# Optimization experiments

Measured on AMD Instinct MI355X. Metric: run time of the kernel, lower is better.

Reference implementation:

```python
import jax, jax.numpy as jnp
import numpy as np

D_MODEL = 1024
D_STATE = 16
D_CONV = 4
EXPAND = 2
DT_RANK = 64
D_INNER = EXPAND * D_MODEL
B, L = 1, 2048


def setup_inputs() -> dict:
    key = jax.random.key(0)
    ks = jax.random.split(key, 10)
    x = jax.random.normal(ks[0], (B, L, D_MODEL), dtype=jnp.float32)
    # linear weights (stored as [out, in], like torch)
    W_in = jax.random.normal(ks[1], (2 * D_INNER, D_MODEL), dtype=jnp.float32) * (1.0 / np.sqrt(D_MODEL))
    conv_w = jax.random.normal(ks[2], (D_INNER, 1, D_CONV), dtype=jnp.float32) * (1.0 / np.sqrt(D_CONV))
    conv_b = jax.random.normal(ks[3], (D_INNER,), dtype=jnp.float32) * 0.02
    W_x = jax.random.normal(ks[4], (DT_RANK + 2 * D_STATE, D_INNER), dtype=jnp.float32) * (1.0 / np.sqrt(D_INNER))
    W_dt = jax.random.normal(ks[5], (D_INNER, DT_RANK), dtype=jnp.float32) * (1.0 / np.sqrt(DT_RANK))
    # dt bias init: inverse-softplus of dt ~ LogUniform(1e-3, 0.1)
    dt = jnp.exp(jax.random.uniform(ks[6], (D_INNER,)) * (np.log(0.1) - np.log(0.001)) + np.log(0.001))
    dt = jnp.clip(dt, 1e-4, None)
    b_dt = dt + jnp.log(-jnp.expm1(-dt))
    # A_log init: log(1..d_state) broadcast over d_inner
    A_log = jnp.log(jnp.broadcast_to(jnp.arange(1, D_STATE + 1, dtype=jnp.float32)[None, :], (D_INNER, D_STATE)))
    D_param = jnp.ones((D_INNER,), dtype=jnp.float32)
    W_out = jax.random.normal(ks[7], (D_MODEL, D_INNER), dtype=jnp.float32) * (1.0 / np.sqrt(D_INNER))
    return dict(x=x, W_in=W_in, conv_w=conv_w, conv_b=conv_b, W_x=W_x,
                W_dt=W_dt, b_dt=b_dt, A_log=A_log, D_param=D_param, W_out=W_out)


def _silu(v):
    return v * jax.nn.sigmoid(v)


def _mamba_forward(x, W_in, conv_w, conv_b, W_x, W_dt, b_dt, A_log, D_param, W_out):
    # in_proj: (B, L, 2*d_inner)
    xz = jnp.einsum('bld,ed->ble', x, W_in)
    x_in, z = jnp.split(xz, 2, axis=-1)  # each (B, L, d_inner)

    # depthwise causal conv1d (torch pads d_conv-1 both sides then truncates -> causal left pad)
    xc = jnp.transpose(x_in, (0, 2, 1))  # (B, d_inner, L)
    xc = jax.lax.conv_general_dilated(
        xc, conv_w,
        window_strides=(1,), padding=[(D_CONV - 1, 0)],
        dimension_numbers=('NCH', 'OIH', 'NCH'),
        feature_group_count=D_INNER)
    xc = xc + conv_b[None, :, None]
    x_conv = _silu(jnp.transpose(xc, (0, 2, 1)))  # (B, L, d_inner)

    # selective SSM
    A = -jnp.exp(A_log)  # (d_inner, d_state)
    x_dbl = jnp.einsum('bld,ed->ble', x_conv, W_x)  # (B, L, dt_rank + 2*d_state)
    dt_low, B_ssm, C = jnp.split(x_dbl, [DT_RANK, DT_RANK + D_STATE], axis=-1)
    dt = jax.nn.softplus(jnp.einsum('blr,dr->bld', dt_low, W_dt) + b_dt)  # (B, L, d_inner)

    dA = jnp.exp(jnp.einsum('bld,dn->bldn', dt, A))                        # (B, L, d_inner, d_state)
    dBx = dt[..., None] * B_ssm[:, :, None, :] * x_conv[..., None]          # dB * x, (B, L, d_inner, d_state)

    def step(h, inp):
        dA_t, dBx_t, C_t = inp          # (B, d, n), (B, d, n), (B, n)
        h = dA_t * h + dBx_t
        y_t = jnp.einsum('bdn,bn->bd', h, C_t)
        return h, y_t

    h0 = jnp.zeros((x.shape[0], D_INNER, D_STATE), dtype=x.dtype)
    xs = (jnp.swapaxes(dA, 0, 1), jnp.swapaxes(dBx, 0, 1), jnp.swapaxes(C, 0, 1))
    _, ys = jax.lax.scan(step, h0, xs)   # ys: (L, B, d_inner)
    y = jnp.swapaxes(ys, 0, 1) + x_conv * D_param  # (B, L, d_inner)

    y = y * _silu(z)
    return jnp.einsum('bld,ed->ble', y, W_out)  # (B, L, d_model)


def reference(x, W_in, conv_w, conv_b, W_x, W_dt, b_dt, A_log, D_param, W_out):
    return _mamba_forward(x, W_in, conv_w, conv_b, W_x, W_dt, b_dt, A_log, D_param, W_out)
```

## Files before the change

kernel.cpp:

```cpp
#include <hip/hip_runtime.h>
#include <math.h>

#define LSEQ   2048
#define DMODEL 1024
#define DINNER 2048
#define DSTATE 16
#define DTRANK 64
#define XCOLS  96
#define CL     32
#define NC     (LSEQ/CL)
#define SSTATE (DINNER*DSTATE)

typedef __attribute__((ext_vector_type(8))) short bf16x8;
typedef __attribute__((ext_vector_type(4))) float f32x4;
typedef unsigned short ushort_t;
typedef unsigned int uint_t;

__device__ __forceinline__ float siluf(float v) { return v / (1.f + __expf(-v)); }

__device__ __forceinline__ ushort_t f2bf(float f) {
    uint_t u = __float_as_uint(f);
    u += 0x7FFFu + ((u >> 16) & 1u);
    return (ushort_t)(u >> 16);
}
__device__ __forceinline__ float bf2f(ushort_t u) {
    return __uint_as_float((uint_t)u << 16);
}

__device__ __forceinline__ bf16x8 cvt8(float4 lo, float4 hi) {
    bf16x8 r;
    r[0] = (short)f2bf(lo.x); r[1] = (short)f2bf(lo.y);
    r[2] = (short)f2bf(lo.z); r[3] = (short)f2bf(lo.w);
    r[4] = (short)f2bf(hi.x); r[5] = (short)f2bf(hi.y);
    r[6] = (short)f2bf(hi.z); r[7] = (short)f2bf(hi.w);
    return r;
}

__global__ __launch_bounds__(256)
void cast6_kernel(const float* __restrict__ s0, ushort_t* __restrict__ d0, int c0,
                  const float* __restrict__ s1, ushort_t* __restrict__ d1, int c1,
                  const float* __restrict__ s2, ushort_t* __restrict__ d2, int c2,
                  const float* __restrict__ s3, ushort_t* __restrict__ d3, int c3,
                  const float* __restrict__ s4, ushort_t* __restrict__ d4, int c4,
                  float* __restrict__ z0, int cz)
{
    int i = (blockIdx.x * 256 + threadIdx.x) * 8;
    int tot = c0 + c1 + c2 + c3 + c4;
    if (i < tot) {
        const float* s; ushort_t* d;
        if (i < c0)                { s = s0 + i;                  d = d0 + i; }
        else if (i < c0+c1)        { s = s1 + (i-c0);             d = d1 + (i-c0); }
        else if (i < c0+c1+c2)     { s = s2 + (i-c0-c1);          d = d2 + (i-c0-c1); }
        else if (i < c0+c1+c2+c3)  { s = s3 + (i-c0-c1-c2);       d = d3 + (i-c0-c1-c2); }
        else                       { s = s4 + (i-c0-c1-c2-c3);    d = d4 + (i-c0-c1-c2-c3); }
        *(bf16x8*)d = cvt8(*(const float4*)s, *(const float4*)(s + 4));
    } else if (i < tot + cz) {
        float* z = z0 + (i - tot);
        *(float4*)z       = make_float4(0.f, 0.f, 0.f, 0.f);
        *(float4*)(z + 4) = make_float4(0.f, 0.f, 0.f, 0.f);
    }
}

__device__ __forceinline__ void stage_tile(const ushort_t* __restrict__ A,
                                           const ushort_t* __restrict__ B,
                                           ushort_t* As, ushort_t* Bs,
                                           int m0, int n0, int K, int k0, int tid)
{
#pragma unroll
    for (int j = 0; j < 2; j++) {
        const int c   = j * 256 + tid;
        const int row = c & 127;
        const int kbi = c >> 7;
        __builtin_amdgcn_global_load_lds(
            (const __attribute__((address_space(1))) uint_t*)(A + (size_t)(m0 + row) * K + k0 + kbi * 8),
            (__attribute__((address_space(3))) uint_t*)((char*)As + c * 16), 16, 0, 0);
        __builtin_amdgcn_global_load_lds(
            (const __attribute__((address_space(1))) uint_t*)(B + (size_t)(n0 + row) * K + k0 + kbi * 8),
            (__attribute__((address_space(3))) uint_t*)((char*)Bs + c * 16), 16, 0, 0);
    }
}

template<int EPI, int SPLITK>
__global__ __launch_bounds__(256)
void gemm_bf16(const ushort_t* __restrict__ A,
               const ushort_t* __restrict__ B,
               float* __restrict__ C,
               ushort_t* __restrict__ Xb,
               ushort_t* __restrict__ Gz,
               int M, int N, int K, size_t partStride)
{
    __shared__ ushort_t As[2][4096];
    __shared__ ushort_t Bs[2][4096];

    const int tid  = threadIdx.x;
    const int wid  = tid >> 6;
    const int lane = tid & 63;
    const int m0 = blockIdx.x * 128;
    const int n0 = blockIdx.y * 128;
    const int kcnt  = K / SPLITK;
    const int kbase = (SPLITK > 1) ? blockIdx.z * kcnt : 0;
    const int NT = kcnt / 32;
    float* Cp = (EPI == 0) ? C + (size_t)blockIdx.z * partStride : C;
    const int wr = (wid >> 1) * 64;
    const int wc = (wid & 1) * 64;
    const int lr = lane & 15;
    const int kbq = lane >> 4;

    f32x4 acc[4][4];
#pragma unroll
    for (int m = 0; m < 4; m++)
#pragma unroll
        for (int n = 0; n < 4; n++)
            acc[m][n] = (f32x4){0.f, 0.f, 0.f, 0.f};

    stage_tile(A, B, As[0], Bs[0], m0, n0, K, kbase, tid);

    for (int t = 0; t < NT; t++) {
        const int cur = t & 1;
        if (t + 1 < NT) {
            stage_tile(A, B, As[cur ^ 1], Bs[cur ^ 1], m0, n0, K, kbase + (t + 1) * 32, tid);
            asm volatile("s_waitcnt vmcnt(4)" ::: "memory");
        } else {
            asm volatile("s_waitcnt vmcnt(0)" ::: "memory");
        }
        __builtin_amdgcn_s_barrier();
        __builtin_amdgcn_sched_barrier(0);

        bf16x8 af[4], bfr[4];
#pragma unroll
        for (int m = 0; m < 4; m++)
            af[m] = *(const bf16x8*)&As[cur][(kbq * 128 + wr + m * 16 + lr) * 8];
#pragma unroll
        for (int n = 0; n < 4; n++)
            bfr[n] = *(const bf16x8*)&Bs[cur][(kbq * 128 + wc + n * 16 + lr) * 8];
#pragma unroll
        for (int m = 0; m < 4; m++)
#pragma unroll
            for (int n = 0; n < 4; n++)
                acc[m][n] = __builtin_amdgcn_mfma_f32_16x16x32_bf16(af[m], bfr[n], acc[m][n], 0, 0, 0);

        __builtin_amdgcn_sched_barrier(0);
        __builtin_amdgcn_s_barrier();
    }

    const int er = (lane >> 4) * 4;
    const int ec = lane & 15;
    if (EPI == 0) {
#pragma unroll
        for (int m = 0; m < 4; m++) {
            const int grow = m0 + wr + m * 16 + er;
#pragma unroll
            for (int n = 0; n < 4; n++) {
                const int gcol = n0 + wc + n * 16 + ec;
#pragma unroll
                for (int r = 0; r < 4; r++)
                    Cp[(size_t)(grow + r) * N + gcol] = acc[m][n][r];
            }
        }
    } else {
        const bool xside = (n0 < DINNER);
#pragma unroll
        for (int m = 0; m < 4; m++) {
            const int grow = m0 + wr + m * 16 + er;
#pragma unroll
            for (int n = 0; n < 4; n++) {
                const int gcol = n0 + wc + n * 16 + ec;
#pragma unroll
                for (int r = 0; r < 4; r++) {
                    float v = acc[m][n][r];
                    if (xside)
                        Xb[(size_t)(grow + r) * DINNER + gcol] = f2bf(v);
                    else
                        Gz[(size_t)(grow + r) * DINNER + (gcol - DINNER)] = f2bf(siluf(v));
                }
            }
        }
    }
}

__global__ __launch_bounds__(256)
void add2_kernel(const float* __restrict__ p0, const float* __restrict__ p1,
                 float* __restrict__ out, int n)
{
    int i = (blockIdx.x * 256 + threadIdx.x) * 4;
    if (i >= n) return;
    float4 a = *(const float4*)(p0 + i);
    float4 b = *(const float4*)(p1 + i);
    *(float4*)(out + i) = make_float4(a.x + b.x, a.y + b.y, a.z + b.z, a.w + b.w);
}

__global__ __launch_bounds__(256)
void gemm_xdbl(const ushort_t* __restrict__ A,
               const ushort_t* __restrict__ B,
               float* __restrict__ Cout)
{
    const int tid = threadIdx.x, wid = tid >> 6, lane = tid & 63;
    const int m0 = blockIdx.x * 128;
    const int kbase = blockIdx.z * 128;
    const int wr = (wid >> 1) * 64;
    const int wc = (wid & 1) * 48;
    const int lr = lane & 15;
    const int kq = (lane >> 4) * 8;

    f32x4 acc[4][3];
#pragma unroll
    for (int m = 0; m < 4; m++)
#pragma unroll
        for (int n = 0; n < 3; n++)
            acc[m][n] = (f32x4){0.f, 0.f, 0.f, 0.f};

#pragma unroll
    for (int ks = 0; ks < 4; ks++) {
        const int k0 = kbase + ks * 32;
        bf16x8 af[4], bfr[3];
#pragma unroll
        for (int m = 0; m < 4; m++)
            af[m] = *(const bf16x8*)(A + (size_t)(m0 + wr + m * 16 + lr) * DINNER + k0 + kq);
#pragma unroll
        for (int n = 0; n < 3; n++)
            bfr[n] = *(const bf16x8*)(B + (size_t)(wc + n * 16 + lr) * DINNER + k0 + kq);
#pragma unroll
        for (int m = 0; m < 4; m++)
#pragma unroll
            for (int n = 0; n < 3; n++)
                acc[m][n] = __builtin_amdgcn_mfma_f32_16x16x32_bf16(af[m], bfr[n], acc[m][n], 0, 0, 0);
    }

    const int er = (lane >> 4) * 4;
    const int ec = lane & 15;
#pragma unroll
    for (int m = 0; m < 4; m++)
#pragma unroll
        for (int n = 0; n < 3; n++)
#pragma unroll
            for (int r = 0; r < 4; r++)
                atomicAdd(&Cout[(size_t)(m0 + wr + m * 16 + er + r) * XCOLS + wc + n * 16 + ec],
                          acc[m][n][r]);
}

__global__ __launch_bounds__(256)
void gemm_dt(const float* __restrict__ Axd,
             const ushort_t* __restrict__ Bw,
             const float* __restrict__ bias,
             ushort_t* __restrict__ dtmb)
{
    const int tid = threadIdx.x, wid = tid >> 6, lane = tid & 63;
    const int m0 = blockIdx.x * 128;
    const int n0 = blockIdx.y * 128;
    const int wr = (wid >> 1) * 64;
    const int wc = (wid & 1) * 64;
    const int lr = lane & 15;
    const int kq = (lane >> 4) * 8;

    f32x4 acc[4][4];
#pragma unroll
    for (int m = 0; m < 4; m++)
#pragma unroll
        for (int n = 0; n < 4; n++)
            acc[m][n] = (f32x4){0.f, 0.f, 0.f, 0.f};

#pragma unroll
    for (int kk = 0; kk < 2; kk++) {
        bf16x8 af[4], bfr[4];
#pragma unroll
        for (int m = 0; m < 4; m++) {
            const float* p = Axd + (size_t)(m0 + wr + m * 16 + lr) * XCOLS + kk * 32 + kq;
            af[m] = cvt8(*(const float4*)p, *(const float4*)(p + 4));
        }
#pragma unroll
        for (int n = 0; n < 4; n++)
            bfr[n] = *(const bf16x8*)(Bw + (size_t)(n0 + wc + n * 16 + lr) * DTRANK + kk * 32 + kq);
#pragma unroll
        for (int m = 0; m < 4; m++)
#pragma unroll
            for (int n = 0; n < 4; n++)
                acc[m][n] = __builtin_amdgcn_mfma_f32_16x16x32_bf16(af[m], bfr[n], acc[m][n], 0, 0, 0);
    }

    const int er = (lane >> 4) * 4;
    const int ec = lane & 15;
#pragma unroll
    for (int m = 0; m < 4; m++)
#pragma unroll
        for (int n = 0; n < 4; n++) {
            const int gcol = n0 + wc + n * 16 + ec;
            const float bv = bias[gcol];
#pragma unroll
            for (int r = 0; r < 4; r++) {
                float c = acc[m][n][r] + bv;
                c = (c > 20.f) ? c : log1pf(__expf(c));
                dtmb[(size_t)(m0 + wr + m * 16 + er + r) * DINNER + gcol] = f2bf(c);
            }
        }
}

__global__ __launch_bounds__(256)
void conv_silu_kernel(const ushort_t* __restrict__ xinb,
                      const float* __restrict__ conv_w,
                      const float* __restrict__ conv_b,
                      ushort_t* __restrict__ xcb)
{
    int idx = blockIdx.x * 256 + threadIdx.x;
    if (idx >= LSEQ * DINNER) return;
    int t = idx / DINNER;
    int d = idx - t * DINNER;
    float acc = conv_b[d];
#pragma unroll
    for (int j = 0; j < 4; j++) {
        int tt = t - 3 + j;
        if (tt >= 0)
            acc = fmaf(conv_w[d*4 + j], bf2f(xinb[(size_t)tt * DINNER + d]), acc);
    }
    xcb[idx] = f2bf(siluf(acc));
}

__global__ __launch_bounds__(256)
void scan_phase1(const ushort_t* __restrict__ dtmb,
                 const float* __restrict__ xdbl,
                 const ushort_t* __restrict__ xcb,
                 const float* __restrict__ A_log,
                 float* __restrict__ Aprod, float* __restrict__ hend)
{
    __shared__ float Bs[CL][16];
    const int tid = threadIdx.x;
    const int d = blockIdx.x * 256 + tid;
    const int c = blockIdx.y;
    const int t0 = c * CL;

    {
        int t = tid >> 3, n = (tid * 2) & 15;
        float2 v = *(const float2*)&xdbl[(size_t)(t0 + t) * XCOLS + DTRANK + n];
        Bs[t][n] = v.x; Bs[t][n + 1] = v.y;
    }

    float a[16];
#pragma unroll
    for (int q = 0; q < 4; q++) {
        f32x4 v = *(const f32x4*)&A_log[(size_t)d * DSTATE + q * 4];
#pragma unroll
        for (int j = 0; j < 4; j++) a[q * 4 + j] = -__expf(v[j]);
    }
    float h[16];
#pragma unroll
    for (int n = 0; n < 16; n++) h[n] = 0.f;
    float sdt = 0.f;

    __syncthreads();

    float dtv = bf2f(dtmb[(size_t)t0 * DINNER + d]);
    float xv  = bf2f(xcb[(size_t)t0 * DINNER + d]);
    for (int tt = 0; tt < CL; tt++) {
        int tn_ = t0 + ((tt + 1 < CL) ? tt + 1 : tt);
        float dtv_n = bf2f(dtmb[(size_t)tn_ * DINNER + d]);
        float xv_n  = bf2f(xcb[(size_t)tn_ * DINNER + d]);

        f32x4 Bq[4];
#pragma unroll
        for (int q = 0; q < 4; q++) Bq[q] = *(const f32x4*)&Bs[tt][q * 4];
        float dtx = dtv * xv;
        sdt += dtv;
#pragma unroll
        for (int n = 0; n < 16; n++) {
            float e = __expf(dtv * a[n]);
            h[n] = fmaf(e, h[n], dtx * Bq[n >> 2][n & 3]);
        }
        dtv = dtv_n; xv = xv_n;
    }

#pragma unroll
    for (int n = 0; n < 16; n++) {
        const size_t k = (size_t)c * SSTATE + (size_t)n * DINNER + d;
        hend[k]  = h[n];
        Aprod[k] = __expf(a[n] * sdt);
    }
}

__global__ __launch_bounds__(256)
void scan_phase2(const float* __restrict__ Aprod, float* __restrict__ hend)
{
    const int idx = blockIdx.x * 256 + threadIdx.x;
    float carry = 0.f;
#pragma unroll
    for (int c = 0; c < NC; c++) {
        const size_t k = (size_t)c * SSTATE + idx;
        float oh = hend[k];
        float oA = Aprod[k];
        hend[k] = carry;
        carry = fmaf(oA, carry, oh);
    }
}

__global__ __launch_bounds__(256)
void scan_phase3(const ushort_t* __restrict__ dtmb,
                 const float* __restrict__ xdbl,
                 const ushort_t* __restrict__ xcb,
                 const float* __restrict__ A_log,
                 const float* __restrict__ Dp,
                 const ushort_t* __restrict__ gz,
                 const float* __restrict__ hinit,
                 ushort_t* __restrict__ yb)
{
    __shared__ float Bs[CL][16];
    __shared__ float Cs[CL][16];
    const int tid = threadIdx.x;
    const int d = blockIdx.x * 256 + tid;
    const int c = blockIdx.y;
    const int t0 = c * CL;

    {
        int r = tid & 127;
        int t = r >> 2, n = (r * 4) & 15;
        const float* src = &xdbl[(size_t)(t0 + t) * XCOLS + DTRANK + ((tid < 128) ? 0 : DSTATE) + n];
        float4 v = *(const float4*)src;
        float* dst = (tid < 128) ? &Bs[t][n] : &Cs[t][n];
        dst[0] = v.x; dst[1] = v.y; dst[2] = v.z; dst[3] = v.w;
    }

    float a[16];
#pragma unroll
    for (int q = 0; q < 4; q++) {
        f32x4 v = *(const f32x4*)&A_log[(size_t)d * DSTATE + q * 4];
#pragma unroll
        for (int j = 0; j < 4; j++) a[q * 4 + j] = -__expf(v[j]);
    }
    const float Dv = Dp[d];
    float h[16];
#pragma unroll
    for (int n = 0; n < 16; n++)
        h[n] = hinit[(size_t)c * SSTATE + (size_t)n * DINNER + d];

    __syncthreads();

    float dtv = bf2f(dtmb[(size_t)t0 * DINNER + d]);
    float xv  = bf2f(xcb[(size_t)t0 * DINNER + d]);
    for (int tt = 0; tt < CL; tt++) {
        const int t = t0 + tt;
        int tn_ = t0 + ((tt + 1 < CL) ? tt + 1 : tt);
        float dtv_n = bf2f(dtmb[(size_t)tn_ * DINNER + d]);
        float xv_n  = bf2f(xcb[(size_t)tn_ * DINNER + d]);
        float gzv   = bf2f(gz[(size_t)t * DINNER + d]);

        f32x4 Bq[4], Cq[4];
#pragma unroll
        for (int q = 0; q < 4; q++) {
            Bq[q] = *(const f32x4*)&Bs[tt][q * 4];
            Cq[q] = *(const f32x4*)&Cs[tt][q * 4];
        }
        float dtx = dtv * xv;
        float y = 0.f;
#pragma unroll
        for (int n = 0; n < 16; n++) {
            float e = __expf(dtv * a[n]);
            h[n] = fmaf(e, h[n], dtx * Bq[n >> 2][n & 3]);
            y = fmaf(h[n], Cq[n >> 2][n & 3], y);
        }
        yb[(size_t)t * DINNER + d] = f2bf((y + Dv * xv) * gzv);
        dtv = dtv_n; xv = xv_n;
    }
}

extern "C" void kernel_launch(void* const* d_in, const int* in_sizes, int n_in,
                              void* d_out, int out_size, void* d_ws, size_t ws_size,
                              hipStream_t stream)
{
    const float* x      = (const float*)d_in[0];
    const float* W_in   = (const float*)d_in[1];
    const float* conv_w = (const float*)d_in[2];
    const float* conv_b = (const float*)d_in[3];
    const float* W_x    = (const float*)d_in[4];
    const float* W_dt   = (const float*)d_in[5];
    const float* b_dt   = (const float*)d_in[6];
    const float* A_log  = (const float*)d_in[7];
    const float* D_par  = (const float*)d_in[8];
    const float* W_out  = (const float*)d_in[9];
    float* out = (float*)d_out;
    float* ws  = (float*)d_ws;

    float* xdbl  = ws;
    float* Aprod = xdbl + (size_t)LSEQ * XCOLS;
    float* hend  = Aprod + (size_t)NC * SSTATE;
    ushort_t* xb   = (ushort_t*)(hend + (size_t)NC * SSTATE);
    ushort_t* Wib  = xb   + (size_t)LSEQ * DMODEL;
    ushort_t* Wob  = Wib  + (size_t)(2*DINNER) * DMODEL;
    ushort_t* Wxb  = Wob  + (size_t)DMODEL * DINNER;
    ushort_t* Wdtb = Wxb  + (size_t)XCOLS * DINNER;
    ushort_t* xinb = Wdtb + (size_t)DINNER * DTRANK;
    ushort_t* gz   = xinb + (size_t)LSEQ * DINNER;
    ushort_t* xcb  = gz   + (size_t)LSEQ * DINNER;
    ushort_t* dtmb = xcb  + (size_t)LSEQ * DINNER;
    ushort_t* yb   = dtmb + (size_t)LSEQ * DINNER;
    float* outp = (float*)xcb;

    {
        int c0 = LSEQ * DMODEL, c1 = 2 * DINNER * DMODEL, c2 = DMODEL * DINNER;
        int c3 = XCOLS * DINNER, c4 = DINNER * DTRANK;
        int cz = LSEQ * XCOLS;
        int total = c0 + c1 + c2 + c3 + c4 + cz;
        hipLaunchKernelGGL(cast6_kernel, dim3((total / 8 + 255) / 256), dim3(256), 0, stream,
                           x, xb, c0, W_in, Wib, c1, W_out, Wob, c2,
                           W_x, Wxb, c3, W_dt, Wdtb, c4, xdbl, cz);
    }

    hipLaunchKernelGGL((gemm_bf16<1,1>), dim3(LSEQ/128, (2*DINNER)/128), dim3(256), 0, stream,
                       xb, Wib, (float*)nullptr, xinb, gz, LSEQ, 2*DINNER, DMODEL, (size_t)0);

    hipLaunchKernelGGL(conv_silu_kernel, dim3((LSEQ*DINNER)/256), dim3(256), 0, stream,
                       xinb, conv_w, conv_b, xcb);

    hipLaunchKernelGGL(gemm_xdbl, dim3(LSEQ/128, 1, 16), dim3(256), 0, stream,
                       xcb, Wxb, xdbl);

    hipLaunchKernelGGL(gemm_dt, dim3(LSEQ/128, DINNER/128), dim3(256), 0, stream,
                       xdbl, Wdtb, b_dt, dtmb);

    hipLaunchKernelGGL(scan_phase1, dim3(DINNER/256, NC), dim3(256), 0, stream,
                       dtmb, xdbl, xcb, A_log, Aprod, hend);
    hipLaunchKernelGGL(scan_phase2, dim3(SSTATE/256), dim3(256), 0, stream,
                       Aprod, hend);
    hipLaunchKernelGGL(scan_phase3, dim3(DINNER/256, NC), dim3(256), 0, stream,
                       dtmb, xdbl, xcb, A_log, D_par, gz, hend, yb);

    hipLaunchKernelGGL((gemm_bf16<0,2>), dim3(LSEQ/128, DMODEL/128, 2), dim3(256), 0, stream,
                       yb, Wob, outp, (ushort_t*)nullptr, (ushort_t*)nullptr,
                       LSEQ, DMODEL, DINNER, (size_t)(LSEQ*DMODEL));
    hipLaunchKernelGGL(add2_kernel, dim3((LSEQ*DMODEL/4)/256), dim3(256), 0, stream,
                       outp, outp + (size_t)LSEQ*DMODEL, out, LSEQ*DMODEL);
}
```

Baseline: 200.0 us.

## Parallelize chunk-carry scan with warp shuffles, lengthen chunks, split-K out_proj by four

Doubles the scan chunk length to 64, which halves the number of chunks to 32. The inter-chunk carry pass changes from a serial per-state loop into a 32-lane warp shuffle scan over packed (A, h) float2 pairs. The output projection switches from split-K=2 to split-K=4 with a generic partial-sum reduction kernel, and its partials move to the xinb buffer. The aim is more parallelism in phase 2 and the out GEMM, at the cost of longer serial loops per thread in phases 1 and 3 and more partial-sum traffic.

```diff
diff --git a/kernel.cpp b/kernel.cpp
--- a/kernel.cpp
+++ b/kernel.cpp
@@ -7,7 +7,7 @@
 #define DSTATE 16
 #define DTRANK 64
 #define XCOLS  96
-#define CL     32
+#define CL     64
 #define NC     (LSEQ/CL)
 #define SSTATE (DINNER*DSTATE)
 
@@ -178,15 +178,19 @@
     }
 }
 
-__global__ __launch_bounds__(256)
-void add2_kernel(const float* __restrict__ p0, const float* __restrict__ p1,
-                 float* __restrict__ out, int n)
+template<int NP>
+__global__ __launch_bounds__(256)
+void addp_kernel(const float* __restrict__ parts, float* __restrict__ out, int n)
 {
     int i = (blockIdx.x * 256 + threadIdx.x) * 4;
     if (i >= n) return;
-    float4 a = *(const float4*)(p0 + i);
-    float4 b = *(const float4*)(p1 + i);
-    *(float4*)(out + i) = make_float4(a.x + b.x, a.y + b.y, a.z + b.z, a.w + b.w);
+    float4 s = *(const float4*)(parts + i);
+#pragma unroll
+    for (int p = 1; p < NP; p++) {
+        float4 v = *(const float4*)(parts + (size_t)p * n + i);
+        s.x += v.x; s.y += v.y; s.z += v.z; s.w += v.w;
+    }
+    *(float4*)(out + i) = s;
 }
 
 __global__ __launch_bounds__(256)
@@ -319,7 +323,7 @@
                  const float* __restrict__ xdbl,
                  const ushort_t* __restrict__ xcb,
                  const float* __restrict__ A_log,
-                 float* __restrict__ Aprod, float* __restrict__ hend)
+                 float2* __restrict__ state)
 {
     __shared__ float Bs[CL][16];
     const int tid = threadIdx.x;
@@ -328,9 +332,9 @@
     const int t0 = c * CL;
 
     {
-        int t = tid >> 3, n = (tid * 2) & 15;
-        float2 v = *(const float2*)&xdbl[(size_t)(t0 + t) * XCOLS + DTRANK + n];
-        Bs[t][n] = v.x; Bs[t][n + 1] = v.y;
+        int t = tid >> 2, n = (tid & 3) * 4;
+        float4 v = *(const float4*)&xdbl[(size_t)(t0 + t) * XCOLS + DTRANK + n];
+        Bs[t][n] = v.x; Bs[t][n+1] = v.y; Bs[t][n+2] = v.z; Bs[t][n+3] = v.w;
     }
 
     float a[16];
@@ -368,26 +372,28 @@
     }
 
 #pragma unroll
-    for (int n = 0; n < 16; n++) {
-        const size_t k = (size_t)c * SSTATE + (size_t)n * DINNER + d;
-        hend[k]  = h[n];
-        Aprod[k] = __expf(a[n] * sdt);
-    }
-}
-
-__global__ __launch_bounds__(256)
-void scan_phase2(const float* __restrict__ Aprod, float* __restrict__ hend)
-{
-    const int idx = blockIdx.x * 256 + threadIdx.x;
-    float carry = 0.f;
-#pragma unroll
-    for (int c = 0; c < NC; c++) {
-        const size_t k = (size_t)c * SSTATE + idx;
-        float oh = hend[k];
-        float oA = Aprod[k];
-        hend[k] = carry;
-        carry = fmaf(oA, carry, oh);
-    }
+    for (int n = 0; n < 16; n++)
+        state[(size_t)c * SSTATE + (size_t)n * DINNER + d] =
+            make_float2(__expf(a[n] * sdt), h[n]);
+}
+
+__global__ __launch_bounds__(256)
+void scan_phase2(float2* __restrict__ state)
+{
+    const int lane32 = threadIdx.x & 31;
+    const int chain  = blockIdx.x * 8 + (threadIdx.x >> 5);
+    const size_t off = (size_t)lane32 * SSTATE + chain;
+    float2 s = state[off];
+    float A = s.x, h = s.y;
+#pragma unroll
+    for (int dlt = 1; dlt < 32; dlt <<= 1) {
+        float Ap = __shfl_up(A, dlt, 32);
+        float hp = __shfl_up(h, dlt, 32);
+        if (lane32 >= dlt) { h = fmaf(A, hp, h); A = A * Ap; }
+    }
+    float carry = __shfl_up(h, 1, 32);
+    if (lane32 == 0) carry = 0.f;
+    ((float*)&state[off])[1] = carry;
 }
 
 __global__ __launch_bounds__(256)
@@ -397,7 +403,7 @@
                  const float* __restrict__ A_log,
                  const float* __restrict__ Dp,
                  const ushort_t* __restrict__ gz,
-                 const float* __restrict__ hinit,
+                 const float2* __restrict__ state,
                  ushort_t* __restrict__ yb)
 {
     __shared__ float Bs[CL][16];
@@ -409,11 +415,13 @@
 
     {
         int r = tid & 127;
-        int t = r >> 2, n = (r * 4) & 15;
-        const float* src = &xdbl[(size_t)(t0 + t) * XCOLS + DTRANK + ((tid < 128) ? 0 : DSTATE) + n];
-        float4 v = *(const float4*)src;
-        float* dst = (tid < 128) ? &Bs[t][n] : &Cs[t][n];
-        dst[0] = v.x; dst[1] = v.y; dst[2] = v.z; dst[3] = v.w;
+        int t = r >> 1, nb = (r & 1) * 8;
+        const float* src = &xdbl[(size_t)(t0 + t) * XCOLS + DTRANK + ((tid < 128) ? 0 : DSTATE) + nb];
+        float* dst = (tid < 128) ? &Bs[t][nb] : &Cs[t][nb];
+        float4 v0 = *(const float4*)src;
+        float4 v1 = *(const float4*)(src + 4);
+        dst[0]=v0.x; dst[1]=v0.y; dst[2]=v0.z; dst[3]=v0.w;
+        dst[4]=v1.x; dst[5]=v1.y; dst[6]=v1.z; dst[7]=v1.w;
     }
 
     float a[16];
@@ -427,7 +435,7 @@
     float h[16];
 #pragma unroll
     for (int n = 0; n < 16; n++)
-        h[n] = hinit[(size_t)c * SSTATE + (size_t)n * DINNER + d];
+        h[n] = state[(size_t)c * SSTATE + (size_t)n * DINNER + d].y;
 
     __syncthreads();
 
@@ -476,10 +484,9 @@
     float* out = (float*)d_out;
     float* ws  = (float*)d_ws;
 
-    float* xdbl  = ws;
-    float* Aprod = xdbl + (size_t)LSEQ * XCOLS;
-    float* hend  = Aprod + (size_t)NC * SSTATE;
-    ushort_t* xb   = (ushort_t*)(hend + (size_t)NC * SSTATE);
+    float*  xdbl  = ws;
+    float2* state = (float2*)(xdbl + (size_t)LSEQ * XCOLS);
+    ushort_t* xb   = (ushort_t*)(state + (size_t)NC * SSTATE);
     ushort_t* Wib  = xb   + (size_t)LSEQ * DMODEL;
     ushort_t* Wob  = Wib  + (size_t)(2*DINNER) * DMODEL;
     ushort_t* Wxb  = Wob  + (size_t)DMODEL * DINNER;
@@ -489,7 +496,7 @@
     ushort_t* xcb  = gz   + (size_t)LSEQ * DINNER;
     ushort_t* dtmb = xcb  + (size_t)LSEQ * DINNER;
     ushort_t* yb   = dtmb + (size_t)LSEQ * DINNER;
-    float* outp = (float*)xcb;
+    float* outp = (float*)xinb;
 
     {
         int c0 = LSEQ * DMODEL, c1 = 2 * DINNER * DMODEL, c2 = DMODEL * DINNER;
@@ -514,15 +521,15 @@
                        xdbl, Wdtb, b_dt, dtmb);
 
     hipLaunchKernelGGL(scan_phase1, dim3(DINNER/256, NC), dim3(256), 0, stream,
-                       dtmb, xdbl, xcb, A_log, Aprod, hend);
-    hipLaunchKernelGGL(scan_phase2, dim3(SSTATE/256), dim3(256), 0, stream,
-                       Aprod, hend);
+                       dtmb, xdbl, xcb, A_log, state);
+    hipLaunchKernelGGL(scan_phase2, dim3(SSTATE/8), dim3(256), 0, stream,
+                       state);
     hipLaunchKernelGGL(scan_phase3, dim3(DINNER/256, NC), dim3(256), 0, stream,
-                       dtmb, xdbl, xcb, A_log, D_par, gz, hend, yb);
-
-    hipLaunchKernelGGL((gemm_bf16<0,2>), dim3(LSEQ/128, DMODEL/128, 2), dim3(256), 0, stream,
+                       dtmb, xdbl, xcb, A_log, D_par, gz, state, yb);
+
+    hipLaunchKernelGGL((gemm_bf16<0,4>), dim3(LSEQ/128, DMODEL/128, 4), dim3(256), 0, stream,
                        yb, Wob, outp, (ushort_t*)nullptr, (ushort_t*)nullptr,
                        LSEQ, DMODEL, DINNER, (size_t)(LSEQ*DMODEL));
-    hipLaunchKernelGGL(add2_kernel, dim3((LSEQ*DMODEL/4)/256), dim3(256), 0, stream,
-                       outp, outp + (size_t)LSEQ*DMODEL, out, LSEQ*DMODEL);
-}
+    hipLaunchKernelGGL((addp_kernel<4>), dim3((LSEQ*DMODEL/4)/256), dim3(256), 0, stream,
+                       outp, out, LSEQ*DMODEL);
+}
```

After: 211.6 us. 1.06x slower.

## Stage GEMM epilogues through LDS for vector stores; interleave scan chunk state

Applied to the files above, without the earlier changes.

The in_proj and dt GEMM epilogues now write bf16 results into swizzled shared memory, then read them back as 8-element rows so global writes are wide, coalesced 16-byte stores instead of scattered 2-byte stores. The separate Aprod and hend arrays for the chunked scan are merged into one interleaved float2 state array, so phase 2 does one 8-byte load per chunk. The out_proj partial buffer is moved onto xinb. The gemm_dt epilogue also keeps a redundant scalar store of zero before each vector store, which adds write traffic. The extra shared-memory round trip and __syncthreads add a small cost per tile.

```diff
diff --git a/kernel.cpp b/kernel.cpp
--- a/kernel.cpp
+++ b/kernel.cpp
@@ -159,21 +159,32 @@
         }
     } else {
         const bool xside = (n0 < DINNER);
-#pragma unroll
-        for (int m = 0; m < 4; m++) {
-            const int grow = m0 + wr + m * 16 + er;
-#pragma unroll
-            for (int n = 0; n < 4; n++) {
-                const int gcol = n0 + wc + n * 16 + ec;
+        ushort_t* eps = (wid < 2) ? As[wid] : Bs[wid - 2];
+#pragma unroll
+        for (int m = 0; m < 4; m++)
+#pragma unroll
+            for (int n = 0; n < 4; n++)
 #pragma unroll
                 for (int r = 0; r < 4; r++) {
+                    const int rl = m * 16 + er + r;
+                    const int cl = n * 16 + ec;
                     float v = acc[m][n][r];
-                    if (xside)
-                        Xb[(size_t)(grow + r) * DINNER + gcol] = f2bf(v);
-                    else
-                        Gz[(size_t)(grow + r) * DINNER + (gcol - DINNER)] = f2bf(siluf(v));
+                    eps[rl * 64 + (cl ^ ((rl & 7) * 8))] =
+                        xside ? f2bf(v) : f2bf(siluf(v));
                 }
-            }
+        __syncthreads();
+        const int row8 = lane >> 3;
+        const int c8   = (lane & 7) * 8;
+#pragma unroll
+        for (int p = 0; p < 8; p++) {
+            const int rl = p * 8 + row8;
+            bf16x8 v = *(const bf16x8*)&eps[rl * 64 + (c8 ^ ((rl & 7) * 8))];
+            const int grow = m0 + wr + rl;
+            const int gcol = n0 + wc + c8;
+            if (xside)
+                *(bf16x8*)(Xb + (size_t)grow * DINNER + gcol) = v;
+            else
+                *(bf16x8*)(Gz + (size_t)grow * DINNER + (gcol - DINNER)) = v;
         }
     }
 }
@@ -244,6 +255,7 @@
              const float* __restrict__ bias,
              ushort_t* __restrict__ dtmb)
 {
+    __shared__ ushort_t eps4[4][4096];
     const int tid = threadIdx.x, wid = tid >> 6, lane = tid & 63;
     const int m0 = blockIdx.x * 128;
     const int n0 = blockIdx.y * 128;
@@ -279,19 +291,31 @@
 
     const int er = (lane >> 4) * 4;
     const int ec = lane & 15;
+    ushort_t* eps = eps4[wid];
 #pragma unroll
     for (int m = 0; m < 4; m++)
 #pragma unroll
         for (int n = 0; n < 4; n++) {
-            const int gcol = n0 + wc + n * 16 + ec;
-            const float bv = bias[gcol];
+            const int cl = n * 16 + ec;
+            const float bv = bias[n0 + wc + cl];
 #pragma unroll
             for (int r = 0; r < 4; r++) {
+                const int rl = m * 16 + er + r;
                 float c = acc[m][n][r] + bv;
                 c = (c > 20.f) ? c : log1pf(__expf(c));
-                dtmb[(size_t)(m0 + wr + m * 16 + er + r) * DINNER + gcol] = f2bf(c);
+                eps[rl * 64 + (cl ^ ((rl & 7) * 8))] = f2bf(c);
             }
         }
+    __syncthreads();
+    const int row8 = lane >> 3;
+    const int c8   = (lane & 7) * 8;
+#pragma unroll
+    for (int p = 0; p < 8; p++) {
+        const int rl = p * 8 + row8;
+        bf16x8 v = *(const bf16x8*)&eps[rl * 64 + (c8 ^ ((rl & 7) * 8))];
+        dtmb[(size_t)(m0 + wr + rl) * DINNER + n0 + wc + c8] = 0;
+        *(bf16x8*)(dtmb + (size_t)(m0 + wr + rl) * DINNER + n0 + wc + c8) = v;
+    }
 }
 
 __global__ __launch_bounds__(256)
@@ -319,7 +343,7 @@
                  const float* __restrict__ xdbl,
                  const ushort_t* __restrict__ xcb,
                  const float* __restrict__ A_log,
-                 float* __restrict__ Aprod, float* __restrict__ hend)
+                 float2* __restrict__ state)
 {
     __shared__ float Bs[CL][16];
     const int tid = threadIdx.x;
@@ -368,25 +392,21 @@
     }
 
 #pragma unroll
-    for (int n = 0; n < 16; n++) {
-        const size_t k = (size_t)c * SSTATE + (size_t)n * DINNER + d;
-        hend[k]  = h[n];
-        Aprod[k] = __expf(a[n] * sdt);
-    }
-}
-
-__global__ __launch_bounds__(256)
-void scan_phase2(const float* __restrict__ Aprod, float* __restrict__ hend)
+    for (int n = 0; n < 16; n++)
+        state[(size_t)c * SSTATE + (size_t)n * DINNER + d] =
+            make_float2(__expf(a[n] * sdt), h[n]);
+}
+
+__global__ __launch_bounds__(256)
+void scan_phase2(float2* __restrict__ state)
 {
     const int idx = blockIdx.x * 256 + threadIdx.x;
     float carry = 0.f;
 #pragma unroll
     for (int c = 0; c < NC; c++) {
-        const size_t k = (size_t)c * SSTATE + idx;
-        float oh = hend[k];
-        float oA = Aprod[k];
-        hend[k] = carry;
-        carry = fmaf(oA, carry, oh);
+        float2 s = state[(size_t)c * SSTATE + idx];
+        ((float*)&state[(size_t)c * SSTATE + idx])[1] = carry;
+        carry = fmaf(s.x, carry, s.y);
     }
 }
 
@@ -397,7 +417,7 @@
                  const float* __restrict__ A_log,
                  const float* __restrict__ Dp,
                  const ushort_t* __restrict__ gz,
-                 const float* __restrict__ hinit,
+                 const float2* __restrict__ state,
                  ushort_t* __restrict__ yb)
 {
     __shared__ float Bs[CL][16];
@@ -427,7 +447,7 @@
     float h[16];
 #pragma unroll
     for (int n = 0; n < 16; n++)
-        h[n] = hinit[(size_t)c * SSTATE + (size_t)n * DINNER + d];
+        h[n] = state[(size_t)c * SSTATE + (size_t)n * DINNER + d].y;
 
     __syncthreads();
 
@@ -476,10 +496,9 @@
     float* out = (float*)d_out;
     float* ws  = (float*)d_ws;
 
-    float* xdbl  = ws;
-    float* Aprod = xdbl + (size_t)LSEQ * XCOLS;
-    float* hend  = Aprod + (size_t)NC * SSTATE;
-    ushort_t* xb   = (ushort_t*)(hend + (size_t)NC * SSTATE);
+    float*  xdbl  = ws;
+    float2* state = (float2*)(xdbl + (size_t)LSEQ * XCOLS);
+    ushort_t* xb   = (ushort_t*)(state + (size_t)NC * SSTATE);
     ushort_t* Wib  = xb   + (size_t)LSEQ * DMODEL;
     ushort_t* Wob  = Wib  + (size_t)(2*DINNER) * DMODEL;
     ushort_t* Wxb  = Wob  + (size_t)DMODEL * DINNER;
@@ -489,7 +508,7 @@
     ushort_t* xcb  = gz   + (size_t)LSEQ * DINNER;
     ushort_t* dtmb = xcb  + (size_t)LSEQ * DINNER;
     ushort_t* yb   = dtmb + (size_t)LSEQ * DINNER;
-    float* outp = (float*)xcb;
+    float* outp = (float*)xinb;
 
     {
         int c0 = LSEQ * DMODEL, c1 = 2 * DINNER * DMODEL, c2 = DMODEL * DINNER;
@@ -514,11 +533,11 @@
                        xdbl, Wdtb, b_dt, dtmb);
 
     hipLaunchKernelGGL(scan_phase1, dim3(DINNER/256, NC), dim3(256), 0, stream,
-                       dtmb, xdbl, xcb, A_log, Aprod, hend);
+                       dtmb, xdbl, xcb, A_log, state);
     hipLaunchKernelGGL(scan_phase2, dim3(SSTATE/256), dim3(256), 0, stream,
-                       Aprod, hend);
+                       state);
     hipLaunchKernelGGL(scan_phase3, dim3(DINNER/256, NC), dim3(256), 0, stream,
-                       dtmb, xdbl, xcb, A_log, D_par, gz, hend, yb);
+                       dtmb, xdbl, xcb, A_log, D_par, gz, state, yb);
 
     hipLaunchKernelGGL((gemm_bf16<0,2>), dim3(LSEQ/128, DMODEL/128, 2), dim3(256), 0, stream,
                        yb, Wob, outp, (ushort_t*)nullptr, (ushort_t*)nullptr,
```

Measured after the change: 203.3 us. Within noise of the previous version (+1.6%).
